# Kernel tuning notes

Measured on AMD Instinct MI355X. Metric: run time of the kernel, lower is better.

The kernel has to match this reference:

```python
import jax, jax.numpy as jnp
import numpy as np

B, S, H, NH = 4, 2048, 256, 8
EPS = 1e-5


def setup_inputs() -> dict:
    key = jax.random.key(0)
    ks = jax.random.split(key, 12)
    p = lambda k, shape: (jax.random.normal(k, shape, jnp.float32) * 0.02)
    return {
        "x": jax.random.normal(ks[0], (B, S, H), jnp.float32),
        "lengths": jax.random.randint(ks[1], (B,), 0, S).astype(jnp.int32),
        "atten_in": jnp.zeros((1,), jnp.float32),
        "Wq": p(ks[2], (H, H)), "bq": jnp.zeros((H,), jnp.float32),
        "Wk": p(ks[3], (H, H)), "bk": jnp.zeros((H,), jnp.float32),
        "Wv": p(ks[4], (H, H)), "bv": jnp.zeros((H,), jnp.float32),
        "W1": p(ks[5], (H, H)), "b1": jnp.zeros((H,), jnp.float32),
        "W2": p(ks[6], (H, H)), "b2": jnp.zeros((H,), jnp.float32),
        "g1": jnp.ones((H,), jnp.float32), "beta1": jnp.zeros((H,), jnp.float32),
        "g2": jnp.ones((H,), jnp.float32), "beta2": jnp.zeros((H,), jnp.float32),
    }


def _layer_norm(x, g, b):
    mu = x.mean(-1, keepdims=True)
    var = ((x - mu) ** 2).mean(-1, keepdims=True)
    return (x - mu) / jnp.sqrt(var + EPS) * g + b


def reference(x, lengths, atten_in, Wq, bq, Wk, bk, Wv, bv, W1, b1, W2, b2, g1, beta1, g2, beta2):
    Bx, Sx, Hx = x.shape
    hd = Hx // NH
    # QKV projections, split heads -> [B, NH, S, hd]
    q = (x @ Wq + bq).reshape(Bx, Sx, NH, hd).transpose(0, 2, 1, 3)
    k = (x @ Wk + bk).reshape(Bx, Sx, NH, hd).transpose(0, 2, 1, 3)
    v = (x @ Wv + bv).reshape(Bx, Sx, NH, hd).transpose(0, 2, 1, 3)
    # NOTE: original scales by sqrt(hidden_size), not sqrt(head_dim)
    scores = jnp.einsum('bhqd,bhkd->bhqk', q, k) / np.sqrt(Hx).astype(np.float32)
    pos = jnp.arange(Sx)
    causal = pos[:, None] >= pos[None, :]                     # [S, S]
    row_ok = pos[None, :] < lengths[:, None]                  # [B, S]: mask query rows >= length
    head_ok = jnp.arange(NH)[None, :] < lengths[:, None]      # [B, NH]: original loop masks heads >= length
    mask = causal[None, None] & row_ok[:, None, :, None] & head_ok[:, :, None, None]
    neg = jnp.finfo(scores.dtype).min
    logits = jnp.where(mask, scores, neg)
    atten = jax.nn.softmax(logits, axis=-1)
    # original: masked_fill((atten > 0) == False, 0) -> fully masked rows (NaN in torch) become 0
    atten = jnp.where(mask, atten, 0.0)
    row_valid = mask.any(-1, keepdims=True)
    atten = jnp.where(row_valid, atten, 0.0)
    out = jnp.einsum('bhqk,bhkd->bhqd', atten, v).transpose(0, 2, 1, 3).reshape(Bx, Sx, Hx)
    atten_mean = atten.mean(axis=1)  # [B, S, S], detached in original
    out_1 = x + out  # dropout p=0 / eval mode -> identity
    out_1_norm = _layer_norm(out_1, g1, beta1)
    ff = jax.nn.gelu(out_1_norm @ W1 + b1, approximate=False) @ W2 + b2
    y_prim = _layer_norm(out_1_norm + ff, g2, beta2)
    return (y_prim, lengths, atten_mean)
```

## Files before the change

### kernel.cpp

```cpp
#include <hip/hip_runtime.h>
#include <math.h>

#define BB 4
#define SS 2048
#define HH 256
#define NHH 8
#define EPSV 1e-5f
#define NC 8
#define CHW (SS/NC)
#define QPRE 0.09016844005556021f

#if __has_builtin(__builtin_amdgcn_exp2f)
#define EXP2F(x) __builtin_amdgcn_exp2f(x)
#else
#define EXP2F(x) __expf((x) * 0.6931471805599453f)
#endif

typedef unsigned short ushortT;
typedef __attribute__((ext_vector_type(8))) short bf16x8;
typedef __attribute__((ext_vector_type(4))) float f32x4;

__device__ inline ushortT f2bf(float f) {
    union { float f; unsigned int u; } x; x.f = f;
    unsigned int r = x.u + 0x7FFFu + ((x.u >> 16) & 1u);
    return (ushortT)(r >> 16);
}
__device__ inline ushortT f2bf_rz(float f) {
    union { float f; unsigned int u; } x; x.f = f;
    return (ushortT)(x.u >> 16);
}
__device__ inline float bf2f(ushortT u) {
    union { unsigned int i; float f; } x; x.i = ((unsigned int)u) << 16;
    return x.f;
}

__global__ __launch_bounds__(256) void prep(const float* __restrict__ x,
        ushortT* __restrict__ xb, const int* __restrict__ L,
        float* __restrict__ out_len,
        const float* __restrict__ Wa, const float* __restrict__ Wb,
        const float* __restrict__ Wc, const float* __restrict__ Wd,
        const float* __restrict__ We, ushortT* __restrict__ Wtb) {
    const int bid = blockIdx.x;
    if (bid < 1024) {
        const int i = (bid * 256 + threadIdx.x) << 3;
        float4 v0 = *(const float4*)(x + i);
        float4 v1 = *(const float4*)(x + i + 4);
        bf16x8 o;
        o[0] = (short)f2bf(v0.x); o[1] = (short)f2bf(v0.y);
        o[2] = (short)f2bf(v0.z); o[3] = (short)f2bf(v0.w);
        o[4] = (short)f2bf(v1.x); o[5] = (short)f2bf(v1.y);
        o[6] = (short)f2bf(v1.z); o[7] = (short)f2bf(v1.w);
        *(bf16x8*)(xb + i) = o;
        if (bid == 0 && threadIdx.x < BB) out_len[threadIdx.x] = (float)L[threadIdx.x];
        return;
    }
    const int wb = bid - 1024;
    const int z = wb >> 6;
    const int rem = wb & 63;
    const int k0 = (rem >> 3) << 5, n0 = (rem & 7) << 5;
    const float* W = (z == 0) ? Wa : (z == 1) ? Wb : (z == 2) ? Wc : (z == 3) ? Wd : We;
    __shared__ float tile[32][33];
    const int t = threadIdx.x;
    const int r = t >> 3, c4 = (t & 7) << 2;
    float4 v = *(const float4*)(W + (size_t)(k0 + r) * HH + n0 + c4);
    tile[r][c4+0] = v.x; tile[r][c4+1] = v.y; tile[r][c4+2] = v.z; tile[r][c4+3] = v.w;
    __syncthreads();
    ushort4 o;
    o.x = f2bf(tile[c4+0][r]); o.y = f2bf(tile[c4+1][r]);
    o.z = f2bf(tile[c4+2][r]); o.w = f2bf(tile[c4+3][r]);
    *(ushort4*)(Wtb + (size_t)z * 65536 + (size_t)(n0 + r) * HH + k0 + c4) = o;
}

__global__ __launch_bounds__(256) void gemm_qkv(const ushortT* __restrict__ A,
        const ushortT* __restrict__ Wtb,
        const float* __restrict__ bq, const float* __restrict__ bk,
        const float* __restrict__ bv,
        ushortT* __restrict__ Qb, ushortT* __restrict__ Kb,
        ushortT* __restrict__ Vt) {
    __shared__ ushortT As[64][264];
    __shared__ ushortT Ws[64][264];
    const int wsel = blockIdx.y >> 2;
    const int n0 = (blockIdx.y & 3) << 6;
    const ushortT* Wt = Wtb + (size_t)wsel * 65536;
    const float* bias = (wsel == 0) ? bq : (wsel == 1) ? bk : bv;
    const int tid = threadIdx.x;
    const int m0 = blockIdx.x << 6;
    #pragma unroll
    for (int t = 0; t < 8; ++t) {
        const int f = t * 256 + tid;
        const int r = f >> 5;
        const int cc = (f & 31) << 3;
        *(bf16x8*)&As[r][cc] = *(const bf16x8*)(A + (size_t)(m0 + r) * HH + cc);
        *(bf16x8*)&Ws[r][cc] = *(const bf16x8*)(Wt + (size_t)(n0 + r) * HH + cc);
    }
    __syncthreads();
    const int w = tid >> 6, lane = tid & 63;
    const int lg = lane >> 4, lc = lane & 15;
    const int wr = (w & 1) << 5, wc = (w >> 1) << 5;
    f32x4 acc[2][2];
    const f32x4 z4 = {0.f, 0.f, 0.f, 0.f};
    acc[0][0] = z4; acc[0][1] = z4; acc[1][0] = z4; acc[1][1] = z4;
    #pragma unroll
    for (int k0 = 0; k0 < 256; k0 += 32) {
        bf16x8 a0 = *(const bf16x8*)&As[wr + lc][k0 + lg*8];
        bf16x8 a1 = *(const bf16x8*)&As[wr + 16 + lc][k0 + lg*8];
        bf16x8 b0 = *(const bf16x8*)&Ws[wc + lc][k0 + lg*8];
        bf16x8 b1 = *(const bf16x8*)&Ws[wc + 16 + lc][k0 + lg*8];
        acc[0][0] = __builtin_amdgcn_mfma_f32_16x16x32_bf16(a0, b0, acc[0][0], 0, 0, 0);
        acc[0][1] = __builtin_amdgcn_mfma_f32_16x16x32_bf16(a0, b1, acc[0][1], 0, 0, 0);
        acc[1][0] = __builtin_amdgcn_mfma_f32_16x16x32_bf16(a1, b0, acc[1][0], 0, 0, 0);
        acc[1][1] = __builtin_amdgcn_mfma_f32_16x16x32_bf16(a1, b1, acc[1][1], 0, 0, 0);
    }
    ushortT* Out = (wsel == 0) ? Qb : Kb;
    #pragma unroll
    for (int RH = 0; RH < 2; ++RH)
        #pragma unroll
        for (int CH = 0; CH < 2; ++CH) {
            const int col = n0 + wc + CH*16 + lc;
            const float bvv = bias[col];
            float v[4];
            #pragma unroll
            for (int r = 0; r < 4; ++r) {
                v[r] = acc[RH][CH][r] + bvv;
                if (wsel == 0) v[r] *= QPRE;
            }
            if (wsel < 2) {
                #pragma unroll
                for (int r = 0; r < 4; ++r) {
                    const int row = m0 + wr + RH*16 + lg*4 + r;
                    Out[(size_t)row * HH + col] = f2bf(v[r]);
                }
            } else {
                const int row0 = m0 + wr + RH*16 + lg*4;
                const int bidx = row0 >> 11, s0 = row0 & (SS - 1);
                ushort4 o;
                o.x = f2bf(v[0]); o.y = f2bf(v[1]); o.z = f2bf(v[2]); o.w = f2bf(v[3]);
                *(ushort4*)(Vt + ((size_t)(bidx * HH + col)) * SS + s0) = o;
            }
        }
}

template<int MODE>
__global__ __launch_bounds__(256) void gemm_mfma(const ushortT* __restrict__ A,
        const ushortT* __restrict__ Wt, const float* __restrict__ bias,
        void* __restrict__ Cv) {
    __shared__ ushortT As[64][264];
    __shared__ ushortT Ws[64][264];
    const int tid = threadIdx.x;
    const int m0 = blockIdx.x << 6;
    const int n0 = blockIdx.y << 6;
    #pragma unroll
    for (int t = 0; t < 8; ++t) {
        const int f = t * 256 + tid;
        const int r = f >> 5;
        const int cc = (f & 31) << 3;
        *(bf16x8*)&As[r][cc] = *(const bf16x8*)(A + (size_t)(m0 + r) * HH + cc);
        *(bf16x8*)&Ws[r][cc] = *(const bf16x8*)(Wt + (size_t)(n0 + r) * HH + cc);
    }
    __syncthreads();
    const int w = tid >> 6, lane = tid & 63;
    const int lg = lane >> 4, lc = lane & 15;
    const int wr = (w & 1) << 5, wc = (w >> 1) << 5;
    f32x4 acc[2][2];
    const f32x4 z4 = {0.f, 0.f, 0.f, 0.f};
    acc[0][0] = z4; acc[0][1] = z4; acc[1][0] = z4; acc[1][1] = z4;
    #pragma unroll
    for (int k0 = 0; k0 < 256; k0 += 32) {
        bf16x8 a0 = *(const bf16x8*)&As[wr + lc][k0 + lg*8];
        bf16x8 a1 = *(const bf16x8*)&As[wr + 16 + lc][k0 + lg*8];
        bf16x8 b0 = *(const bf16x8*)&Ws[wc + lc][k0 + lg*8];
        bf16x8 b1 = *(const bf16x8*)&Ws[wc + 16 + lc][k0 + lg*8];
        acc[0][0] = __builtin_amdgcn_mfma_f32_16x16x32_bf16(a0, b0, acc[0][0], 0, 0, 0);
        acc[0][1] = __builtin_amdgcn_mfma_f32_16x16x32_bf16(a0, b1, acc[0][1], 0, 0, 0);
        acc[1][0] = __builtin_amdgcn_mfma_f32_16x16x32_bf16(a1, b0, acc[1][0], 0, 0, 0);
        acc[1][1] = __builtin_amdgcn_mfma_f32_16x16x32_bf16(a1, b1, acc[1][1], 0, 0, 0);
    }
    #pragma unroll
    for (int RH = 0; RH < 2; ++RH)
        #pragma unroll
        for (int CH = 0; CH < 2; ++CH) {
            const int col = n0 + wc + CH*16 + lc;
            const float bv = bias[col];
            #pragma unroll
            for (int r = 0; r < 4; ++r) {
                const int row = m0 + wr + RH*16 + lg*4 + r;
                float v = acc[RH][CH][r] + bv;
                if (MODE == 2) v = 0.5f * v * (1.0f + erff(v * 0.70710678118f));
                if (MODE == 0) ((float*)Cv)[(size_t)row * HH + col] = v;
                else           ((ushortT*)Cv)[(size_t)row * HH + col] = f2bf(v);
            }
        }
}

__global__ __launch_bounds__(512) void attn_sums(const ushortT* __restrict__ Qb,
        const ushortT* __restrict__ Kb, const int* __restrict__ lengths,
        float* __restrict__ Psum) {
    const int b = blockIdx.z, c = blockIdx.y;
    const int i0 = blockIdx.x << 5;
    const int len = lengths[b];
    const int jmax = min(i0 + 31, len - 1);
    const int jstart = c * CHW;
    if (i0 >= len || jstart > jmax) return;
    const int tid = threadIdx.x;
    const int w = tid >> 6, lane = tid & 63;
    const int lg = lane >> 4, lc = lane & 15;
    bf16x8 qf[2];
    #pragma unroll
    for (int RH = 0; RH < 2; ++RH)
        qf[RH] = *(const bf16x8*)(Qb + ((size_t)(b * SS + i0 + RH*16 + lc)) * HH + w*32 + lg*8);
    const f32x4 z4 = {0.f, 0.f, 0.f, 0.f};
    float lsum[2][4] = {};
    const int jend = min(jstart + CHW - 32, (jmax >> 5) << 5);
    bf16x8 kf0 = *(const bf16x8*)(Kb + ((size_t)(b * SS + jstart + lc)) * HH + w*32 + lg*8);
    bf16x8 kf1 = *(const bf16x8*)(Kb + ((size_t)(b * SS + jstart + 16 + lc)) * HH + w*32 + lg*8);
    for (int j0 = jstart; j0 <= jend; j0 += 32) {
        bf16x8 ck0 = kf0, ck1 = kf1;
        if (j0 + 32 <= jend) {
            kf0 = *(const bf16x8*)(Kb + ((size_t)(b * SS + j0 + 32 + lc)) * HH + w*32 + lg*8);
            kf1 = *(const bf16x8*)(Kb + ((size_t)(b * SS + j0 + 48 + lc)) * HH + w*32 + lg*8);
        }
        f32x4 s[2][2];
        #pragma unroll
        for (int RH = 0; RH < 2; ++RH) {
            s[RH][0] = __builtin_amdgcn_mfma_f32_16x16x32_bf16(qf[RH], ck0, z4, 0, 0, 0);
            s[RH][1] = __builtin_amdgcn_mfma_f32_16x16x32_bf16(qf[RH], ck1, z4, 0, 0, 0);
        }
        if (j0 < i0) {
            #pragma unroll
            for (int RH = 0; RH < 2; ++RH)
                #pragma unroll
                for (int r = 0; r < 4; ++r)
                    #pragma unroll
                    for (int CH = 0; CH < 2; ++CH)
                        lsum[RH][r] += EXP2F(s[RH][CH][r]);
        } else {
            #pragma unroll
            for (int RH = 0; RH < 2; ++RH)
                #pragma unroll
                for (int r = 0; r < 4; ++r) {
                    const int row = i0 + RH*16 + lg*4 + r;
                    #pragma unroll
                    for (int CH = 0; CH < 2; ++CH) {
                        const int j = j0 + CH*16 + lc;
                        lsum[RH][r] += (j <= row) ? EXP2F(s[RH][CH][r]) : 0.f;
                    }
                }
        }
    }
    #pragma unroll
    for (int RH = 0; RH < 2; ++RH)
        #pragma unroll
        for (int r = 0; r < 4; ++r) {
            float v = lsum[RH][r];
            v += __shfl_xor(v, 1); v += __shfl_xor(v, 2);
            v += __shfl_xor(v, 4); v += __shfl_xor(v, 8);
            if (lc == 0)
                Psum[((size_t)(c * BB + b) * NHH + w) * SS + i0 + RH*16 + lg*4 + r] = v;
        }
}

__global__ __launch_bounds__(256) void attn_reduce(const float* __restrict__ Psum,
        const int* __restrict__ lengths, float* __restrict__ inv) {
    const int idx = blockIdx.x * 256 + threadIdx.x;
    const int b = idx >> 14;
    const int h = (idx >> 11) & 7;
    const int row = idx & (SS - 1);
    const int len = lengths[b];
    float r = 0.f;
    if (row < len && h < len) {
        float s = 0.f;
        const int ncv = (row >> 8) + 1;
        for (int c = 0; c < ncv; ++c)
            s += Psum[((size_t)(c * BB + b) * NHH + h) * SS + row];
        r = (s > 0.f) ? 1.0f / s : 0.f;
    }
    inv[idx] = r;
}

__global__ __launch_bounds__(512) void attn_pv(const ushortT* __restrict__ Qb,
        const ushortT* __restrict__ Kb, const ushortT* __restrict__ Vt,
        const int* __restrict__ lengths, const float* __restrict__ invp,
        ushortT* __restrict__ OPart, float* __restrict__ out_mean) {
    __shared__ __align__(16) ushortT Pb[2][NHH][32][40];
    const int b = blockIdx.z, c = blockIdx.y;
    const int i0 = blockIdx.x << 5;
    const int len = lengths[b];
    const int tid = threadIdx.x;
    const int mr = tid >> 4, mc = (tid & 15) << 1;
    float* meanrow = out_mean + ((size_t)(b * SS + i0 + mr)) * SS + c * CHW + mc;
    const int jmax = min(i0 + 31, len - 1);
    const int jstart = c * CHW;
    const bool act = (i0 < len) && (jstart <= jmax);
    if (!act) {
        #pragma unroll
        for (int jt = 0; jt < CHW; jt += 32)
            *(float2*)(meanrow + jt) = make_float2(0.f, 0.f);
        return;
    }
    const int w = tid >> 6, lane = tid & 63;
    const int lg = lane >> 4, lc = lane & 15;
    bf16x8 qf[2];
    #pragma unroll
    for (int RH = 0; RH < 2; ++RH)
        qf[RH] = *(const bf16x8*)(Qb + ((size_t)(b * SS + i0 + RH*16 + lc)) * HH + w*32 + lg*8);
    float invv[2][4];
    #pragma unroll
    for (int RH = 0; RH < 2; ++RH)
        #pragma unroll
        for (int r = 0; r < 4; ++r)
            invv[RH][r] = invp[((size_t)b * NHH + w) * SS + i0 + RH*16 + lg*4 + r];
    float invh8[NHH];
    #pragma unroll
    for (int hh = 0; hh < NHH; ++hh)
        invh8[hh] = invp[((size_t)b * NHH + hh) * SS + i0 + mr] * 0.125f;
    const f32x4 z4 = {0.f, 0.f, 0.f, 0.f};
    f32x4 O[2][2];
    O[0][0] = z4; O[0][1] = z4; O[1][0] = z4; O[1][1] = z4;
    const int jend = min(jstart + CHW - 32, (jmax >> 5) << 5);
    bf16x8 kf0 = *(const bf16x8*)(Kb + ((size_t)(b * SS + jstart + lc)) * HH + w*32 + lg*8);
    bf16x8 kf1 = *(const bf16x8*)(Kb + ((size_t)(b * SS + jstart + 16 + lc)) * HH + w*32 + lg*8);
    bf16x8 vf0 = *(const bf16x8*)(Vt + ((size_t)(b * HH + w*32 + lc)) * SS + jstart + lg*8);
    bf16x8 vf1 = *(const bf16x8*)(Vt + ((size_t)(b * HH + w*32 + 16 + lc)) * SS + jstart + lg*8);
    int par = 0;
    for (int j0 = jstart; j0 < jstart + CHW; j0 += 32) {
        if (j0 <= jend) {
            bf16x8 ck0 = kf0, ck1 = kf1, cv0 = vf0, cv1 = vf1;
            if (j0 + 32 <= jend) {
                kf0 = *(const bf16x8*)(Kb + ((size_t)(b * SS + j0 + 32 + lc)) * HH + w*32 + lg*8);
                kf1 = *(const bf16x8*)(Kb + ((size_t)(b * SS + j0 + 48 + lc)) * HH + w*32 + lg*8);
                vf0 = *(const bf16x8*)(Vt + ((size_t)(b * HH + w*32 + lc)) * SS + j0 + 32 + lg*8);
                vf1 = *(const bf16x8*)(Vt + ((size_t)(b * HH + w*32 + 16 + lc)) * SS + j0 + 32 + lg*8);
            }
            f32x4 s[2][2];
            #pragma unroll
            for (int RH = 0; RH < 2; ++RH) {
                s[RH][0] = __builtin_amdgcn_mfma_f32_16x16x32_bf16(qf[RH], ck0, z4, 0, 0, 0);
                s[RH][1] = __builtin_amdgcn_mfma_f32_16x16x32_bf16(qf[RH], ck1, z4, 0, 0, 0);
            }
            if (j0 < i0) {
                #pragma unroll
                for (int RH = 0; RH < 2; ++RH)
                    #pragma unroll
                    for (int CH = 0; CH < 2; ++CH)
                        #pragma unroll
                        for (int r = 0; r < 4; ++r)
                            Pb[par][w][RH*16 + lg*4 + r][CH*16 + lc] =
                                f2bf_rz(EXP2F(s[RH][CH][r]));
            } else {
                #pragma unroll
                for (int RH = 0; RH < 2; ++RH)
                    #pragma unroll
                    for (int CH = 0; CH < 2; ++CH)
                        #pragma unroll
                        for (int r = 0; r < 4; ++r) {
                            const int row = i0 + RH*16 + lg*4 + r;
                            const int j = j0 + CH*16 + lc;
                            Pb[par][w][RH*16 + lg*4 + r][CH*16 + lc] =
                                (j <= row) ? f2bf_rz(EXP2F(s[RH][CH][r])) : (ushortT)0;
                        }
            }
            __syncthreads();
            #pragma unroll
            for (int RH = 0; RH < 2; ++RH) {
                bf16x8 pa = *(const bf16x8*)&Pb[par][w][RH*16 + lc][lg*8];
                O[RH][0] = __builtin_amdgcn_mfma_f32_16x16x32_bf16(pa, cv0, O[RH][0], 0, 0, 0);
                O[RH][1] = __builtin_amdgcn_mfma_f32_16x16x32_bf16(pa, cv1, O[RH][1], 0, 0, 0);
            }
            float m0 = 0.f, m1 = 0.f;
            #pragma unroll
            for (int ww = 0; ww < NHH; ++ww) {
                ushort2 t2 = *(const ushort2*)&Pb[par][ww][mr][mc];
                m0 += bf2f(t2.x) * invh8[ww]; m1 += bf2f(t2.y) * invh8[ww];
            }
            *(float2*)(meanrow + (j0 - jstart)) = make_float2(m0, m1);
            par ^= 1;
        } else {
            *(float2*)(meanrow + (j0 - jstart)) = make_float2(0.f, 0.f);
        }
    }
    ushortT* op = OPart + (size_t)c * ((size_t)BB * SS * HH);
    #pragma unroll
    for (int RH = 0; RH < 2; ++RH)
        #pragma unroll
        for (int DH = 0; DH < 2; ++DH)
            #pragma unroll
            for (int r = 0; r < 4; ++r)
                op[((size_t)(b * SS + i0 + RH*16 + lg*4 + r)) * HH + w*32 + DH*16 + lc] =
                    f2bf(O[RH][DH][r] * invv[RH][r]);
}

__global__ __launch_bounds__(256) void add_ln_attn(const float* __restrict__ x,
        const ushortT* __restrict__ OPart, const int* __restrict__ lengths,
        const float* __restrict__ g, const float* __restrict__ beta,
        float* __restrict__ out, ushortT* __restrict__ outb) {
    const int row = blockIdx.x;
    const int c = threadIdx.x;
    const int i = row & (SS - 1);
    const int len = lengths[row >> 11];
    const size_t base = (size_t)row * 256;
    float v = x[base + c];
    if (i < len) {
        const int ncv = (i >> 8) + 1;
        for (int cc = 0; cc < ncv; ++cc)
            v += bf2f(OPart[(size_t)cc * ((size_t)BB * SS * HH) + base + c]);
    }
    __shared__ float red[8];
    float s = v;
    #pragma unroll
    for (int o = 32; o; o >>= 1) s += __shfl_down(s, o, 64);
    const int wid = c >> 6, lane = c & 63;
    if (lane == 0) red[wid] = s;
    __syncthreads();
    float mu = (red[0] + red[1] + red[2] + red[3]) * 0.00390625f;
    float d = v - mu;
    float q = d * d;
    #pragma unroll
    for (int o = 32; o; o >>= 1) q += __shfl_down(q, o, 64);
    if (lane == 0) red[4 + wid] = q;
    __syncthreads();
    float var = (red[4] + red[5] + red[6] + red[7]) * 0.00390625f;
    float res = d * rsqrtf(var + EPSV) * g[c] + beta[c];
    out[base + c] = res;
    outb[base + c] = f2bf(res);
}

__global__ __launch_bounds__(256) void add_ln(const float* __restrict__ A,
        const float* __restrict__ Bv, const float* __restrict__ g,
        const float* __restrict__ beta, float* __restrict__ out) {
    const int row = blockIdx.x;
    const int c = threadIdx.x;
    const size_t base = (size_t)row * 256;
    float v = A[base + c] + Bv[base + c];
    __shared__ float red[8];
    float s = v;
    #pragma unroll
    for (int o = 32; o; o >>= 1) s += __shfl_down(s, o, 64);
    const int wid = c >> 6, lane = c & 63;
    if (lane == 0) red[wid] = s;
    __syncthreads();
    float mu = (red[0] + red[1] + red[2] + red[3]) * 0.00390625f;
    float d = v - mu;
    float q = d * d;
    #pragma unroll
    for (int o = 32; o; o >>= 1) q += __shfl_down(q, o, 64);
    if (lane == 0) red[4 + wid] = q;
    __syncthreads();
    float var = (red[4] + red[5] + red[6] + red[7]) * 0.00390625f;
    out[base + c] = d * rsqrtf(var + EPSV) * g[c] + beta[c];
}

extern "C" void kernel_launch(void* const* d_in, const int* in_sizes, int n_in,
                              void* d_out, int out_size, void* d_ws, size_t ws_size,
                              hipStream_t stream) {
    const float* x   = (const float*)d_in[0];
    const int* lengths = (const int*)d_in[1];
    const float* Wq  = (const float*)d_in[3];
    const float* bq  = (const float*)d_in[4];
    const float* Wk  = (const float*)d_in[5];
    const float* bk  = (const float*)d_in[6];
    const float* Wv  = (const float*)d_in[7];
    const float* bv  = (const float*)d_in[8];
    const float* W1  = (const float*)d_in[9];
    const float* b1  = (const float*)d_in[10];
    const float* W2  = (const float*)d_in[11];
    const float* b2  = (const float*)d_in[12];
    const float* g1  = (const float*)d_in[13];
    const float* be1 = (const float*)d_in[14];
    const float* g2  = (const float*)d_in[15];
    const float* be2 = (const float*)d_in[16];
    float* out = (float*)d_out;
    float* ws  = (float*)d_ws;

    const size_t NELT = (size_t)BB * SS * HH;
    const size_t M1 = 1024 * 1024;

    ushortT* xb  = (ushortT*)ws;
    float*   Psum = ws;
    ushortT* Qbf = (ushortT*)(ws + M1);
    ushortT* Kbf = (ushortT*)(ws + 2 * M1);
    ushortT* Vtb = (ushortT*)(ws + 3 * M1);
    float*   X1N  = ws + 4 * M1;
    ushortT* Wtb = (ushortT*)(ws + 6 * M1);
    float*   inv = ws + 6 * M1 + 262144;
    ushortT* OPart = (ushortT*)(ws + 7 * M1);
    ushortT* X1Nb = (ushortT*)ws;
    ushortT* F1b  = (ushortT*)(ws + M1);
    float*   F2   = ws + 2 * M1;

    float* out_y    = out;
    float* out_len  = out + NELT;
    float* out_mean = out + NELT + 4;

    prep<<<1344, 256, 0, stream>>>(x, xb, lengths, out_len, Wq, Wk, Wv, W1, W2, Wtb);
    gemm_qkv<<<dim3(128, 12), 256, 0, stream>>>(xb, Wtb, bq, bk, bv, Qbf, Kbf, Vtb);
    attn_sums<<<dim3(64, NC, 4), 512, 0, stream>>>(Qbf, Kbf, lengths, Psum);
    attn_reduce<<<256, 256, 0, stream>>>(Psum, lengths, inv);
    attn_pv<<<dim3(64, NC, 4), 512, 0, stream>>>(Qbf, Kbf, Vtb, lengths, inv, OPart, out_mean);
    add_ln_attn<<<8192, 256, 0, stream>>>(x, OPart, lengths, g1, be1, X1N, X1Nb);
    gemm_mfma<2><<<dim3(128, 4), 256, 0, stream>>>(X1Nb, Wtb + 3 * 65536, b1, (void*)F1b);
    gemm_mfma<0><<<dim3(128, 4), 256, 0, stream>>>(F1b,  Wtb + 4 * 65536, b2, (void*)F2);
    add_ln<<<8192, 256, 0, stream>>>(X1N, F2, g2, be2, out_y);
}
```

Measured before the change: 107.8 us.

## Fuse softmax-denominator reduction into attn_pv and cut PV key chunks to two

Drops the separate attn_reduce kernel. Each attn_pv block now reduces the partial exp sums for its 32 rows and 8 heads into shared memory before starting work. The PV pass also splits keys into 2 chunks instead of 8, so each block loops over up to 1024 keys, and add_ln_attn reads and sums fewer bf16 partial-output buffers. This saves a launch plus the partial-buffer traffic, but leaves fewer, longer and more unevenly loaded blocks under the causal mask, which lowers parallelism.

```diff
diff --git a/kernel.cpp b/kernel.cpp
--- a/kernel.cpp
+++ b/kernel.cpp
@@ -8,6 +8,8 @@
 #define EPSV 1e-5f
 #define NC 8
 #define CHW (SS/NC)
+#define NCO 2
+#define CHWO (SS/NCO)
 #define QPRE 0.09016844005556021f
 
 #if __has_builtin(__builtin_amdgcn_exp2f)
@@ -259,44 +261,40 @@
         }
 }
 
-__global__ __launch_bounds__(256) void attn_reduce(const float* __restrict__ Psum,
-        const int* __restrict__ lengths, float* __restrict__ inv) {
-    const int idx = blockIdx.x * 256 + threadIdx.x;
-    const int b = idx >> 14;
-    const int h = (idx >> 11) & 7;
-    const int row = idx & (SS - 1);
-    const int len = lengths[b];
-    float r = 0.f;
-    if (row < len && h < len) {
-        float s = 0.f;
-        const int ncv = (row >> 8) + 1;
-        for (int c = 0; c < ncv; ++c)
-            s += Psum[((size_t)(c * BB + b) * NHH + h) * SS + row];
-        r = (s > 0.f) ? 1.0f / s : 0.f;
-    }
-    inv[idx] = r;
-}
-
 __global__ __launch_bounds__(512) void attn_pv(const ushortT* __restrict__ Qb,
         const ushortT* __restrict__ Kb, const ushortT* __restrict__ Vt,
-        const int* __restrict__ lengths, const float* __restrict__ invp,
+        const int* __restrict__ lengths, const float* __restrict__ Psum,
         ushortT* __restrict__ OPart, float* __restrict__ out_mean) {
     __shared__ __align__(16) ushortT Pb[2][NHH][32][40];
-    const int b = blockIdx.z, c = blockIdx.y;
+    __shared__ float invS[NHH][32];
+    const int b = blockIdx.z, cg = blockIdx.y;
     const int i0 = blockIdx.x << 5;
     const int len = lengths[b];
     const int tid = threadIdx.x;
     const int mr = tid >> 4, mc = (tid & 15) << 1;
-    float* meanrow = out_mean + ((size_t)(b * SS + i0 + mr)) * SS + c * CHW + mc;
+    float* meanrow = out_mean + ((size_t)(b * SS + i0 + mr)) * SS + cg * CHWO + mc;
     const int jmax = min(i0 + 31, len - 1);
-    const int jstart = c * CHW;
+    const int jstart = cg * CHWO;
     const bool act = (i0 < len) && (jstart <= jmax);
     if (!act) {
         #pragma unroll
-        for (int jt = 0; jt < CHW; jt += 32)
+        for (int jt = 0; jt < CHWO; jt += 32)
             *(float2*)(meanrow + jt) = make_float2(0.f, 0.f);
         return;
     }
+    if (tid < NHH * 32) {
+        const int hh = tid >> 5, row = i0 + (tid & 31);
+        float rv = 0.f;
+        if (row < len && hh < len) {
+            float s = 0.f;
+            const int ncv = (row >> 8) + 1;
+            for (int c2 = 0; c2 < ncv; ++c2)
+                s += Psum[((size_t)(c2 * BB + b) * NHH + hh) * SS + row];
+            rv = (s > 0.f) ? 1.0f / s : 0.f;
+        }
+        invS[hh][tid & 31] = rv;
+    }
+    __syncthreads();
     const int w = tid >> 6, lane = tid & 63;
     const int lg = lane >> 4, lc = lane & 15;
     bf16x8 qf[2];
@@ -308,21 +306,21 @@
     for (int RH = 0; RH < 2; ++RH)
         #pragma unroll
         for (int r = 0; r < 4; ++r)
-            invv[RH][r] = invp[((size_t)b * NHH + w) * SS + i0 + RH*16 + lg*4 + r];
+            invv[RH][r] = invS[w][RH*16 + lg*4 + r];
     float invh8[NHH];
     #pragma unroll
     for (int hh = 0; hh < NHH; ++hh)
-        invh8[hh] = invp[((size_t)b * NHH + hh) * SS + i0 + mr] * 0.125f;
+        invh8[hh] = invS[hh][mr] * 0.125f;
     const f32x4 z4 = {0.f, 0.f, 0.f, 0.f};
     f32x4 O[2][2];
     O[0][0] = z4; O[0][1] = z4; O[1][0] = z4; O[1][1] = z4;
-    const int jend = min(jstart + CHW - 32, (jmax >> 5) << 5);
+    const int jend = min(jstart + CHWO - 32, (jmax >> 5) << 5);
     bf16x8 kf0 = *(const bf16x8*)(Kb + ((size_t)(b * SS + jstart + lc)) * HH + w*32 + lg*8);
     bf16x8 kf1 = *(const bf16x8*)(Kb + ((size_t)(b * SS + jstart + 16 + lc)) * HH + w*32 + lg*8);
     bf16x8 vf0 = *(const bf16x8*)(Vt + ((size_t)(b * HH + w*32 + lc)) * SS + jstart + lg*8);
     bf16x8 vf1 = *(const bf16x8*)(Vt + ((size_t)(b * HH + w*32 + 16 + lc)) * SS + jstart + lg*8);
     int par = 0;
-    for (int j0 = jstart; j0 < jstart + CHW; j0 += 32) {
+    for (int j0 = jstart; j0 < jstart + CHWO; j0 += 32) {
         if (j0 <= jend) {
             bf16x8 ck0 = kf0, ck1 = kf1, cv0 = vf0, cv1 = vf1;
             if (j0 + 32 <= jend) {
@@ -378,7 +376,7 @@
             *(float2*)(meanrow + (j0 - jstart)) = make_float2(0.f, 0.f);
         }
     }
-    ushortT* op = OPart + (size_t)c * ((size_t)BB * SS * HH);
+    ushortT* op = OPart + (size_t)cg * ((size_t)BB * SS * HH);
     #pragma unroll
     for (int RH = 0; RH < 2; ++RH)
         #pragma unroll
@@ -400,7 +398,7 @@
     const size_t base = (size_t)row * 256;
     float v = x[base + c];
     if (i < len) {
-        const int ncv = (i >> 8) + 1;
+        const int ncv = (i >> 10) + 1;
         for (int cc = 0; cc < ncv; ++cc)
             v += bf2f(OPart[(size_t)cc * ((size_t)BB * SS * HH) + base + c]);
     }
@@ -481,7 +479,6 @@
     ushortT* Vtb = (ushortT*)(ws + 3 * M1);
     float*   X1N  = ws + 4 * M1;
     ushortT* Wtb = (ushortT*)(ws + 6 * M1);
-    float*   inv = ws + 6 * M1 + 262144;
     ushortT* OPart = (ushortT*)(ws + 7 * M1);
     ushortT* X1Nb = (ushortT*)ws;
     ushortT* F1b  = (ushortT*)(ws + M1);
@@ -494,8 +491,7 @@
     prep<<<1344, 256, 0, stream>>>(x, xb, lengths, out_len, Wq, Wk, Wv, W1, W2, Wtb);
     gemm_qkv<<<dim3(128, 12), 256, 0, stream>>>(xb, Wtb, bq, bk, bv, Qbf, Kbf, Vtb);
     attn_sums<<<dim3(64, NC, 4), 512, 0, stream>>>(Qbf, Kbf, lengths, Psum);
-    attn_reduce<<<256, 256, 0, stream>>>(Psum, lengths, inv);
-    attn_pv<<<dim3(64, NC, 4), 512, 0, stream>>>(Qbf, Kbf, Vtb, lengths, inv, OPart, out_mean);
+    attn_pv<<<dim3(64, NCO, 4), 512, 0, stream>>>(Qbf, Kbf, Vtb, lengths, Psum, OPart, out_mean);
     add_ln_attn<<<8192, 256, 0, stream>>>(x, OPart, lengths, g1, be1, X1N, X1Nb);
     gemm_mfma<2><<<dim3(128, 4), 256, 0, stream>>>(X1Nb, Wtb + 3 * 65536, b1, (void*)F1b);
     gemm_mfma<0><<<dim3(128, 4), 256, 0, stream>>>(F1b,  Wtb + 4 * 65536, b2, (void*)F2);
```

Result: slower. 115.0 us (+6.6%).
